# Kernel tuning notes

Measured on AMD Instinct MI355X. Metric: run time of the kernel, lower is better.

The kernel has to match this reference:

```python
import jax, jax.numpy as jnp
import numpy as np

N = 50000      # nodes
F_IN = 500     # input features
H1, C1 = 4, 32 # layer1 heads, channels (hidden)
H2, C2 = 1, 40 # layer2 heads, channels (num_classes)
E_RAW = 250000 # random edges before self loops
SLOPE = 0.2    # leaky relu negative slope


def _build_edges():
    """1-hop edges with self loops (remove_self_loops+add_self_loops) and
    unique 2-hop edges (nonzeros of adj @ adj), as ints. Deterministic."""
    rng = np.random.RandomState(0)
    src = rng.randint(0, N, E_RAW)
    dst = (src + 1 + rng.randint(0, N - 1, E_RAW)) % N  # no self loops by construction
    sl = np.arange(N)
    src1 = np.concatenate([src, sl])
    dst1 = np.concatenate([dst, sl])
    # CSR by source for 2-hop expansion
    order = np.argsort(src1, kind='stable')
    dst_sorted = dst1[order]
    deg = np.bincount(src1, minlength=N)
    ptr = np.concatenate([[0], np.cumsum(deg)])
    rep = deg[dst1]                      # continuations per edge (a,b) = outdeg(b)
    total = int(rep.sum())
    base = np.repeat(np.cumsum(rep) - rep, rep)
    off = np.arange(total) - base
    starts = np.repeat(ptr[dst1], rep)
    cont = dst_sorted[starts + off]
    two_src = np.repeat(src1, rep)
    key = two_src.astype(np.int64) * N + cont.astype(np.int64)
    uk = np.unique(key)                  # dense_to_sparse keeps unique nonzero positions
    e2 = np.stack([uk // N, uk % N]).astype(np.int32)
    e1 = np.stack([src1, dst1]).astype(np.int32)
    return e1, e2


def _glorot(k, shape):
    fan_in = int(np.prod(shape[:-1]))
    fan_out = int(shape[-1])
    lim = float(np.sqrt(6.0 / (fan_in + fan_out)))
    return jax.random.uniform(k, shape, jnp.float32, -lim, lim)


def setup_inputs() -> dict:
    key = jax.random.key(0)
    ks = jax.random.split(key, 13)
    e1, e2 = _build_edges()
    return {
        'x': jax.random.normal(ks[0], (N, F_IN), jnp.float32),
        'edge_index1': jnp.asarray(e1),
        'edge_index2': jnp.asarray(e2),
        'W_src1': _glorot(ks[1], (F_IN, H1 * C1)),
        'W_dst1': _glorot(ks[2], (F_IN, H1 * C1)),
        'W_dst21': _glorot(ks[3], (F_IN, H1 * C1)),
        'a_src1': _glorot(ks[4], (1, H1, C1)),
        'a_dst1': _glorot(ks[5], (1, H1, C1)),
        'a_dst21': _glorot(ks[6], (1, H1, C1)),
        'W_src2': _glorot(ks[7], (2 * H1 * C1, H2 * C2)),
        'W_dst2': _glorot(ks[8], (2 * H1 * C1, H2 * C2)),
        'W_dst22': _glorot(ks[9], (2 * H1 * C1, H2 * C2)),
        'a_src2': _glorot(ks[10], (1, H2, C2)),
        'a_dst2': _glorot(ks[11], (1, H2, C2)),
        'a_dst22': _glorot(ks[12], (1, H2, C2)),
    }


def _propagate(e, x_src, al_src, al_dst, n):
    """Edge gather -> leaky-relu score -> segment softmax by dst -> scatter-add."""
    s, d = e[0], e[1]
    a = al_src[s] + al_dst[d]                      # [E, H]
    a = jnp.where(a > 0, a, SLOPE * a)             # leaky relu
    amax = jax.lax.stop_gradient(jax.ops.segment_max(a, d, num_segments=n))
    a = jnp.exp(a - amax[d])
    denom = jax.ops.segment_sum(a, d, num_segments=n)
    a = a / (denom[d] + 1e-16)                     # PyG softmax epsilon
    msg = x_src[s] * a[:, :, None]                 # [E, H, C]
    return jax.ops.segment_sum(msg, d, num_segments=n)


def _gat_prop(x, e1, e2, Ws, Wd, Wd2, a_s, a_d, a_d2, H, C, concat, n):
    xs = (x @ Ws).reshape(n, H, C)
    xd = (x @ Wd).reshape(n, H, C)
    xd2 = (x @ Wd2).reshape(n, H, C)
    al_s = (xs * a_s).sum(-1)    # [N, H]
    al_d = (xd * a_d).sum(-1)
    al_d2 = (xd2 * a_d2).sum(-1)
    out = _propagate(e1, xs, al_s, al_d, n)    # 1-hop
    out2 = _propagate(e2, xs, al_s, al_d2, n)  # 2-hop
    if concat:
        out = out.reshape(n, H * C)
        out2 = out2.reshape(n, H * C)
    else:
        out = out.mean(1)
        out2 = out2.mean(1)
    return jnp.concatenate([out, out2], axis=-1)


def reference(x, edge_index1, edge_index2,
              W_src1, W_dst1, W_dst21, a_src1, a_dst1, a_dst21,
              W_src2, W_dst2, W_dst22, a_src2, a_dst2, a_dst22):
    n = x.shape[0]
    h = _gat_prop(x, edge_index1, edge_index2, W_src1, W_dst1, W_dst21,
                  a_src1, a_dst1, a_dst21, H1, C1, True, n)
    h = jax.nn.elu(h)
    h = _gat_prop(h, edge_index1, edge_index2, W_src2, W_dst2, W_dst22,
                  a_src2, a_dst2, a_dst22, H2, C2, False, n)
    return jax.nn.log_softmax(h, axis=1)
```

## Files before the change

kernel.cpp:

```cpp
#include <hip/hip_runtime.h>
#include <hip/hip_bf16.h>
#include <math.h>

typedef unsigned short u16;
typedef unsigned int u32;
typedef unsigned char u8;
typedef __attribute__((ext_vector_type(8))) short short8;
typedef __attribute__((ext_vector_type(4))) float f32x4;
typedef __attribute__((ext_vector_type(2))) float f32x2;

#define NB 128

static __device__ __forceinline__ u16 f2bf(float f) {
    u32 u = __float_as_uint(f);
    u32 r = (u + 0x7fffu + ((u >> 16) & 1u)) >> 16;
    return (u16)r;
}
static __device__ __forceinline__ float bl(u32 u) { return __uint_as_float(u << 16); }
static __device__ __forceinline__ float bh(u32 u) { return __uint_as_float(u & 0xffff0000u); }


__global__ __launch_bounds__(256) void k_bhist(const int* __restrict__ dst, int E,
                                               int* __restrict__ bcnt) {
    __shared__ int lh[NB];
    int tid = threadIdx.x;
    int base = blockIdx.x * 2048;
    for (int i = tid; i < NB; i += 256) lh[i] = 0;
    __syncthreads();
    int cnt = min(2048, E - base);
    #pragma unroll
    for (int k = 0; k < 8; k++) {
        int i = tid + k * 256;
        if (i < cnt) atomicAdd(&lh[dst[base + i] >> 9], 1);
    }
    __syncthreads();
    for (int i = tid; i < NB; i += 256) {
        int c = lh[i];
        if (c) atomicAdd(&bcnt[i], c);
    }
}

__global__ void k_bscan(const int* __restrict__ bcnt, int* __restrict__ bbase,
                        int* __restrict__ bcur, int* __restrict__ ptrN, int nb) {
    __shared__ int sh[NB];
    int t = threadIdx.x;
    int v = (t < nb) ? bcnt[t] : 0;
    sh[t] = v;
    __syncthreads();
    for (int off = 1; off < NB; off <<= 1) {
        int val = sh[t];
        int add = (t >= off) ? sh[t - off] : 0;
        __syncthreads();
        sh[t] = val + add;
        __syncthreads();
    }
    int excl = sh[t] - v;
    if (t <= nb) bbase[t] = excl;
    if (t < nb) bcur[t] = excl;
    if (t == nb) *ptrN = excl;
}

__global__ __launch_bounds__(256) void k_part(const int* __restrict__ src,
                                              const int* __restrict__ dst, int E,
                                              int* __restrict__ bcur,
                                              u32* __restrict__ part) {
    __shared__ int lh[NB];
    __shared__ int gb[NB];
    int tid = threadIdx.x;
    int base = blockIdx.x * 2048;
    for (int i = tid; i < NB; i += 256) lh[i] = 0;
    __syncthreads();
    int cnt = min(2048, E - base);
    int bkt[8], rank[8]; u32 pk[8];
    #pragma unroll
    for (int k = 0; k < 8; k++) {
        int i = tid + k * 256;
        if (i < cnt) {
            int s = src[base + i], d = dst[base + i];
            int b = d >> 9;
            bkt[k] = b;
            pk[k] = ((u32)(d & 511) << 16) | (u32)s;
            rank[k] = atomicAdd(&lh[b], 1);
        } else bkt[k] = -1;
    }
    __syncthreads();
    for (int i = tid; i < NB; i += 256) {
        int c = lh[i];
        gb[i] = c ? atomicAdd(&bcur[i], c) : 0;
    }
    __syncthreads();
    #pragma unroll
    for (int k = 0; k < 8; k++)
        if (bkt[k] >= 0) part[gb[bkt[k]] + rank[k]] = pk[k];
}

__global__ __launch_bounds__(256) void k_dhs(const u32* __restrict__ part,
                                             const int* __restrict__ bbase,
                                             int* __restrict__ ptrArr,
                                             u16* __restrict__ csr, int n) {
    __shared__ int hist[512];
    __shared__ int tsum[256];
    int b = blockIdx.x;
    int t = threadIdx.x;
    int lo = bbase[b], hi = bbase[b + 1];
    hist[t] = 0; hist[t + 256] = 0;
    __syncthreads();
    for (int i = lo + t; i < hi; i += 256)
        atomicAdd(&hist[(part[i] >> 16) & 511], 1);
    __syncthreads();
    int v0 = hist[2 * t], v1 = hist[2 * t + 1];
    tsum[t] = v0 + v1;
    __syncthreads();
    for (int off = 1; off < 256; off <<= 1) {
        int val = tsum[t];
        int add = (t >= off) ? tsum[t - off] : 0;
        __syncthreads();
        tsum[t] = val + add;
        __syncthreads();
    }
    int basep = lo + ((t == 0) ? 0 : tsum[t - 1]);
    int i0 = (b << 9) + 2 * t;
    if (i0 < n)     ptrArr[i0] = basep;
    if (i0 + 1 < n) ptrArr[i0 + 1] = basep + v0;
    __syncthreads();
    hist[2 * t] = basep;
    hist[2 * t + 1] = basep + v0;
    __syncthreads();
    for (int i = lo + t; i < hi; i += 256) {
        u32 pk = part[i];
        int pos = atomicAdd(&hist[(pk >> 16) & 511], 1);
        csr[pos] = (u16)(pk & 0xffffu);
    }
}

__global__ void k_build_Bt1(const float* __restrict__ Ws, const float* __restrict__ Wd,
                            const float* __restrict__ Wd2, const float* __restrict__ as_,
                            const float* __restrict__ ad, const float* __restrict__ ad2,
                            u16* __restrict__ Bt) {
    int t = blockIdx.x * blockDim.x + threadIdx.x;
    if (t >= 144 * 512) return;
    int nn = t >> 9, k = t & 511;
    float v = 0.f;
    if (k < 500) {
        if (nn < 128) v = Ws[k * 128 + nn];
        else if (nn < 140) {
            int q = nn - 128; int h = q & 3;
            const float* W; const float* a;
            if (q < 4)      { W = Ws;  a = as_; }
            else if (q < 8) { W = Wd;  a = ad;  }
            else            { W = Wd2; a = ad2; }
            float s = 0.f;
            #pragma unroll 8
            for (int c = 0; c < 32; c++) s += W[k * 128 + h * 32 + c] * a[h * 32 + c];
            v = s;
        }
    }
    Bt[t] = f2bf(v);
}

__global__ void k_build_Bt2(const float* __restrict__ Ws, const float* __restrict__ Wd,
                            const float* __restrict__ Wd2, const float* __restrict__ as_,
                            const float* __restrict__ ad, const float* __restrict__ ad2,
                            u16* __restrict__ Bt) {
    int t = blockIdx.x * blockDim.x + threadIdx.x;
    if (t >= 48 * 256) return;
    int nn = t >> 8, k = t & 255;
    float v = 0.f;
    if (nn < 40) v = Ws[k * 40 + nn];
    else if (nn < 43) {
        const float* a = (nn == 40) ? as_ : (nn == 41) ? ad : ad2;
        const float* W = Ws;
        if (nn == 41) W = Wd; else if (nn == 42) W = Wd2;
        float s = 0.f;
        #pragma unroll 8
        for (int c = 0; c < 40; c++) s += W[k * 40 + c] * a[c];
        v = s;
    }
    Bt[t] = f2bf(v);
}

__global__ __launch_bounds__(256) void k_mgemm1(const float* __restrict__ A,
                                                const u16* __restrict__ Bt,
                                                u8* __restrict__ xb,
                                                float* __restrict__ alb, int M) {
    __shared__ __align__(16) u16 Bs[144][136];
    int tid = threadIdx.x;
    int wv = tid >> 6, lane = tid & 63;
    int l15 = lane & 15, k8 = lane >> 4;
    int wid = blockIdx.x * 4 + wv;
    int nw = (M + 15) >> 4;
    bool active = wid < nw;
    int rowBlk = wid * 16;
    int arow = rowBlk + l15;
    bool rowOK = active && (arow < M);
    const float* Ap0 = A + (size_t)arow * 500;

    f32x4 acc[9];
    #pragma unroll
    for (int t = 0; t < 9; t++) acc[t] = (f32x4){0.f, 0.f, 0.f, 0.f};

    for (int q = 0; q < 4; q++) {
        if (q) __syncthreads();
        for (int idx = tid; idx < 2304; idx += 256) {
            int row = idx >> 4, c = (idx & 15) * 8;
            *(uint4*)&Bs[row][c] = *(const uint4*)&Bt[row * 512 + q * 128 + c];
        }
        __syncthreads();
        #pragma unroll
        for (int ki = 0; ki < 4; ki++) {
            int kg = q * 128 + ki * 32 + k8 * 8;
            float v[8];
            if (rowOK && (kg + 8 <= 500)) {
                float4 p0 = *(const float4*)(Ap0 + kg);
                float4 p1 = *(const float4*)(Ap0 + kg + 4);
                v[0] = p0.x; v[1] = p0.y; v[2] = p0.z; v[3] = p0.w;
                v[4] = p1.x; v[5] = p1.y; v[6] = p1.z; v[7] = p1.w;
            } else {
                #pragma unroll
                for (int i = 0; i < 8; i++)
                    v[i] = (rowOK && kg + i < 500) ? Ap0[kg + i] : 0.f;
            }
            short8 af;
            ((u32*)&af)[0] = (u32)f2bf(v[0]) | ((u32)f2bf(v[1]) << 16);
            ((u32*)&af)[1] = (u32)f2bf(v[2]) | ((u32)f2bf(v[3]) << 16);
            ((u32*)&af)[2] = (u32)f2bf(v[4]) | ((u32)f2bf(v[5]) << 16);
            ((u32*)&af)[3] = (u32)f2bf(v[6]) | ((u32)f2bf(v[7]) << 16);
            int kl = ki * 32 + k8 * 8;
            #pragma unroll
            for (int t = 0; t < 9; t++) {
                short8 bf = *(const short8*)&Bs[t * 16 + l15][kl];
                acc[t] = __builtin_amdgcn_mfma_f32_16x16x32_bf16(af, bf, acc[t], 0, 0, 0);
            }
        }
    }
    if (active) {
        #pragma unroll
        for (int t = 0; t < 9; t++) {
            #pragma unroll
            for (int rr = 0; rr < 4; rr++) {
                int grow = rowBlk + k8 * 4 + rr;
                if (grow < M) {
                    if (t < 8) {
                        u32 p8 = __builtin_amdgcn_cvt_pk_fp8_f32(acc[t][rr], acc[t][rr], 0, false);
                        xb[(size_t)grow * 128 + t * 16 + l15] = (u8)(p8 & 0xffu);
                    } else if (l15 < 12) {
                        alb[(size_t)grow * 16 + l15] = acc[t][rr];
                    }
                }
            }
        }
    }
}

__global__ __launch_bounds__(256) void k_mgemm2(const u16* __restrict__ A,
                                                const u16* __restrict__ Bt,
                                                u16* __restrict__ xb,
                                                float* __restrict__ alb, int M) {
    __shared__ __align__(16) u16 Bs[48][264];
    int tid = threadIdx.x;
    int wv = tid >> 6, lane = tid & 63;
    int l15 = lane & 15, k8 = lane >> 4;
    int wid = blockIdx.x * 4 + wv;
    int nw = (M + 15) >> 4;
    bool active = wid < nw;
    int rowBlk = wid * 16;
    int arow = rowBlk + l15;
    bool rowOK = active && (arow < M);
    const u16* Ap0 = A + (size_t)arow * 256;

    for (int idx = tid; idx < 1536; idx += 256) {
        int row = idx >> 5, c = (idx & 31) * 8;
        *(uint4*)&Bs[row][c] = *(const uint4*)&Bt[row * 256 + c];
    }
    __syncthreads();

    f32x4 acc[3];
    #pragma unroll
    for (int t = 0; t < 3; t++) acc[t] = (f32x4){0.f, 0.f, 0.f, 0.f};

    #pragma unroll
    for (int ki = 0; ki < 8; ki++) {
        int k0 = ki * 32 + k8 * 8;
        short8 af = {0, 0, 0, 0, 0, 0, 0, 0};
        if (rowOK) af = *(const short8*)(Ap0 + k0);
        #pragma unroll
        for (int t = 0; t < 3; t++) {
            short8 bf = *(const short8*)&Bs[t * 16 + l15][k0];
            acc[t] = __builtin_amdgcn_mfma_f32_16x16x32_bf16(af, bf, acc[t], 0, 0, 0);
        }
    }
    if (active) {
        #pragma unroll
        for (int t = 0; t < 3; t++) {
            #pragma unroll
            for (int rr = 0; rr < 4; rr++) {
                int grow = rowBlk + k8 * 4 + rr;
                if (grow < M) {
                    int col = t * 16 + l15;
                    if (col < 40) xb[(size_t)grow * 40 + col] = f2bf(acc[t][rr]);
                    else if (col < 43) alb[(size_t)grow * 4 + (col - 40)] = acc[t][rr];
                }
            }
        }
    }
}

__global__ __launch_bounds__(256) void k_prop1(const int* __restrict__ ptr, const u16* __restrict__ csr,
                                               const float* __restrict__ al, int doff,
                                               const uint2* __restrict__ xb2v,
                                               u16* __restrict__ out, int n) {
    __shared__ int sbuf[4][64];
    __shared__ __align__(16) float wbuf[4][64][4];
    int tid = threadIdx.x;
    int wv = tid >> 6, lane = tid & 63;
    int wid = (blockIdx.x * 256 + tid) >> 6;
    if (wid >= n) return;
    int b = ptr[wid], e = ptr[wid + 1];
    float4 adv = *(const float4*)(al + (size_t)wid * 16 + doff);
    int l4 = lane & 15, q = lane >> 4;
    int h = l4 >> 2;

    float acc0 = 0.f, acc1 = 0.f, acc2 = 0.f, acc3 = 0.f;
    float acc4 = 0.f, acc5 = 0.f, acc6 = 0.f, acc7 = 0.f;
    float dn0 = 0.f, dn1 = 0.f, dn2 = 0.f, dn3 = 0.f;

    for (int cb = b; cb < e; cb += 64) {
        int cnt = min(64, e - cb);
        int s = 0;
        float w0 = 0.f, w1 = 0.f, w2 = 0.f, w3 = 0.f;
        if (lane < cnt) {
            s = csr[cb + lane];
            float4 av = *(const float4*)(al + (size_t)s * 16);
            float a0 = av.x + adv.x; a0 = a0 > 0.f ? a0 : 0.2f * a0; w0 = __expf(a0);
            float a1 = av.y + adv.y; a1 = a1 > 0.f ? a1 : 0.2f * a1; w1 = __expf(a1);
            float a2 = av.z + adv.z; a2 = a2 > 0.f ? a2 : 0.2f * a2; w2 = __expf(a2);
            float a3 = av.w + adv.w; a3 = a3 > 0.f ? a3 : 0.2f * a3; w3 = __expf(a3);
        }
        dn0 += w0; dn1 += w1; dn2 += w2; dn3 += w3;
        sbuf[wv][lane] = s;
        float4 wq4; wq4.x = w0; wq4.y = w1; wq4.z = w2; wq4.w = w3;
        *(float4*)&wbuf[wv][lane][0] = wq4;
        #pragma unroll 2
        for (int j = 0; j < cnt; j += 4) {
            int jq = j + q;
            int sj = sbuf[wv][jq];
            float wj = wbuf[wv][jq][h];
            uint2 pk = xb2v[(size_t)sj * 16 + l4];
            f32x2 c01 = __builtin_amdgcn_cvt_pk_f32_fp8(pk.x, false);
            f32x2 c23 = __builtin_amdgcn_cvt_pk_f32_fp8(pk.x, true);
            f32x2 c45 = __builtin_amdgcn_cvt_pk_f32_fp8(pk.y, false);
            f32x2 c67 = __builtin_amdgcn_cvt_pk_f32_fp8(pk.y, true);
            acc0 = fmaf(wj, c01.x, acc0);
            acc1 = fmaf(wj, c01.y, acc1);
            acc2 = fmaf(wj, c23.x, acc2);
            acc3 = fmaf(wj, c23.y, acc3);
            acc4 = fmaf(wj, c45.x, acc4);
            acc5 = fmaf(wj, c45.y, acc5);
            acc6 = fmaf(wj, c67.x, acc6);
            acc7 = fmaf(wj, c67.y, acc7);
        }
    }
    acc0 += __shfl_xor(acc0, 16); acc0 += __shfl_xor(acc0, 32);
    acc1 += __shfl_xor(acc1, 16); acc1 += __shfl_xor(acc1, 32);
    acc2 += __shfl_xor(acc2, 16); acc2 += __shfl_xor(acc2, 32);
    acc3 += __shfl_xor(acc3, 16); acc3 += __shfl_xor(acc3, 32);
    acc4 += __shfl_xor(acc4, 16); acc4 += __shfl_xor(acc4, 32);
    acc5 += __shfl_xor(acc5, 16); acc5 += __shfl_xor(acc5, 32);
    acc6 += __shfl_xor(acc6, 16); acc6 += __shfl_xor(acc6, 32);
    acc7 += __shfl_xor(acc7, 16); acc7 += __shfl_xor(acc7, 32);
    #pragma unroll
    for (int o = 32; o > 0; o >>= 1) {
        dn0 += __shfl_xor(dn0, o);
        dn1 += __shfl_xor(dn1, o);
        dn2 += __shfl_xor(dn2, o);
        dn3 += __shfl_xor(dn3, o);
    }
    if (lane < 16) {
        float dh = (h == 0) ? dn0 : (h == 1) ? dn1 : (h == 2) ? dn2 : dn3;
        float inv = 1.f / (dh + 1e-16f);
        float r0 = acc0 * inv, r1 = acc1 * inv, r2 = acc2 * inv, r3 = acc3 * inv;
        float r4 = acc4 * inv, r5 = acc5 * inv, r6 = acc6 * inv, r7 = acc7 * inv;
        r0 = r0 > 0.f ? r0 : __expf(r0) - 1.f;
        r1 = r1 > 0.f ? r1 : __expf(r1) - 1.f;
        r2 = r2 > 0.f ? r2 : __expf(r2) - 1.f;
        r3 = r3 > 0.f ? r3 : __expf(r3) - 1.f;
        r4 = r4 > 0.f ? r4 : __expf(r4) - 1.f;
        r5 = r5 > 0.f ? r5 : __expf(r5) - 1.f;
        r6 = r6 > 0.f ? r6 : __expf(r6) - 1.f;
        r7 = r7 > 0.f ? r7 : __expf(r7) - 1.f;
        uint4 st;
        st.x = (u32)f2bf(r0) | ((u32)f2bf(r1) << 16);
        st.y = (u32)f2bf(r2) | ((u32)f2bf(r3) << 16);
        st.z = (u32)f2bf(r4) | ((u32)f2bf(r5) << 16);
        st.w = (u32)f2bf(r6) | ((u32)f2bf(r7) << 16);
        *(uint4*)(out + (size_t)wid * 256 + l4 * 8) = st;
    }
}

__global__ __launch_bounds__(256) void k_prop2(const int* __restrict__ ptr, const u16* __restrict__ csr,
                                               const float* __restrict__ al, int didx,
                                               const uint2* __restrict__ xbv,
                                               float* __restrict__ out, int n) {
    __shared__ int2 swb[4][64];
    int tid = threadIdx.x;
    int wv = tid >> 6, lane = tid & 63;
    int wid = (blockIdx.x * 256 + tid) >> 6;
    if (wid >= n) return;
    int b = ptr[wid], e = ptr[wid + 1];
    float ad = al[(size_t)wid * 4 + didx];
    int g = lane / 10;
    int cp = lane - g * 10;
    bool act = g < 6;

    float acc0 = 0.f, acc1 = 0.f, acc2 = 0.f, acc3 = 0.f;
    float den = 0.f;

    for (int cb = b; cb < e; cb += 64) {
        int cnt = min(64, e - cb);
        int s = 0; float w = 0.f;
        if (lane < cnt) {
            s = csr[cb + lane];
            float a = al[(size_t)s * 4] + ad;
            a = a > 0.f ? a : 0.2f * a;
            w = __expf(a);
        }
        den += w;
        swb[wv][lane] = make_int2(s, __float_as_int(w));
        #pragma unroll 2
        for (int j = 0; j < cnt; j += 6) {
            int jj = j + g;
            bool valid = act && (jj < cnt);
            int2 sw = swb[wv][valid ? jj : 0];
            float wj = valid ? __int_as_float(sw.y) : 0.f;
            uint2 pk = xbv[(size_t)sw.x * 10 + cp];
            acc0 = fmaf(wj, bl(pk.x), acc0);
            acc1 = fmaf(wj, bh(pk.x), acc1);
            acc2 = fmaf(wj, bl(pk.y), acc2);
            acc3 = fmaf(wj, bh(pk.y), acc3);
        }
    }
    float t0;
    t0 = acc0 + __shfl(acc0, (lane + 30) & 63); acc0 = t0 + __shfl(t0, (lane + 10) & 63) + __shfl(t0, (lane + 20) & 63);
    t0 = acc1 + __shfl(acc1, (lane + 30) & 63); acc1 = t0 + __shfl(t0, (lane + 10) & 63) + __shfl(t0, (lane + 20) & 63);
    t0 = acc2 + __shfl(acc2, (lane + 30) & 63); acc2 = t0 + __shfl(t0, (lane + 10) & 63) + __shfl(t0, (lane + 20) & 63);
    t0 = acc3 + __shfl(acc3, (lane + 30) & 63); acc3 = t0 + __shfl(t0, (lane + 10) & 63) + __shfl(t0, (lane + 20) & 63);
    #pragma unroll
    for (int o = 32; o > 0; o >>= 1) den += __shfl_xor(den, o);
    if (lane < 10) {
        float inv = 1.f / (den + 1e-16f);
        float4 st; st.x = acc0 * inv; st.y = acc1 * inv; st.z = acc2 * inv; st.w = acc3 * inv;
        *(float4*)(out + (size_t)wid * 80 + 4 * cp) = st;
    }
}

__global__ __launch_bounds__(256) void k_lsm(const float* __restrict__ h2, float* __restrict__ out, int n) {
    int wid = (blockIdx.x * blockDim.x + threadIdx.x) >> 6;
    int lane = threadIdx.x & 63;
    if (wid >= n) return;
    const float* row = h2 + (size_t)wid * 80;
    float v0 = row[lane];
    float v1 = (lane < 16) ? row[64 + lane] : -INFINITY;
    float m = fmaxf(v0, v1);
    for (int o = 32; o > 0; o >>= 1) m = fmaxf(m, __shfl_xor(m, o));
    float s = __expf(v0 - m) + ((lane < 16) ? __expf(v1 - m) : 0.f);
    for (int o = 32; o > 0; o >>= 1) s += __shfl_xor(s, o);
    float ls = m + logf(s);
    out[(size_t)wid * 80 + lane] = v0 - ls;
    if (lane < 16) out[(size_t)wid * 80 + 64 + lane] = v1 - ls;
}


extern "C" void kernel_launch(void* const* d_in, const int* in_sizes, int n_in,
                              void* d_out, int out_size, void* d_ws, size_t ws_size,
                              hipStream_t stream) {
    const float* x       = (const float*)d_in[0];
    const int*   e1      = (const int*)d_in[1];
    const int*   e2      = (const int*)d_in[2];
    const float* W_src1  = (const float*)d_in[3];
    const float* W_dst1  = (const float*)d_in[4];
    const float* W_dst21 = (const float*)d_in[5];
    const float* a_src1  = (const float*)d_in[6];
    const float* a_dst1  = (const float*)d_in[7];
    const float* a_dst21 = (const float*)d_in[8];
    const float* W_src2  = (const float*)d_in[9];
    const float* W_dst2  = (const float*)d_in[10];
    const float* W_dst22 = (const float*)d_in[11];
    const float* a_src2  = (const float*)d_in[12];
    const float* a_dst2  = (const float*)d_in[13];
    const float* a_dst22 = (const float*)d_in[14];
    float* out = (float*)d_out;

    const int FIN = 500;
    int n  = in_sizes[0] / FIN;
    int E1 = in_sizes[1] / 2;
    int E2 = in_sizes[2] / 2;
    const int* src1 = e1, *dst1 = e1 + E1;
    const int* src2 = e2, *dst2 = e2 + E2;
    int nb = (n + 511) >> 9;

    char* w = (char*)d_ws;
    auto alloc = [&](size_t bytes) -> char* {
        char* p = w; w += (bytes + 255) & ~(size_t)255; return p;
    };
    u8*    xb1  = (u8*)alloc((size_t)n * 128);
    float* alb1 = (float*)alloc((size_t)n * 16 * 4);
    u16*   hbuf = (u16*)alloc((size_t)n * 256 * 2);
    u16*   xb2  = (u16*)alloc((size_t)n * 40 * 2);
    float* alb2 = (float*)alloc((size_t)n * 4 * 4);
    float* h2   = (float*)alloc((size_t)n * 80 * 4);
    u16*   Bt1  = (u16*)alloc(144 * 512 * 2);
    u16*   Bt2  = (u16*)alloc(48 * 256 * 2);
    int* ptr1 = (int*)alloc((size_t)(n + 1) * 4);
    u16* csr1 = (u16*)alloc((size_t)E1 * 2);
    int* ptr2 = (int*)alloc((size_t)(n + 1) * 4);
    u16* csr2 = (u16*)alloc((size_t)E2 * 2);
    int* bcnt1  = (int*)alloc(NB * 4);
    int* bcnt2  = (int*)alloc(NB * 4);
    int* bbase1 = (int*)alloc((NB + 1) * 4);
    int* bbase2 = (int*)alloc((NB + 1) * 4);
    int* bcur1  = (int*)alloc(NB * 4);
    int* bcur2  = (int*)alloc(NB * 4);
    u32* part2 = (u32*)h2;
    u32* part1 = part2 + E2;

    hipMemsetAsync(bcnt1, 0, NB * 4, stream);
    hipMemsetAsync(bcnt2, 0, NB * 4, stream);
    k_bhist<<<(E1 + 2047) / 2048, 256, 0, stream>>>(dst1, E1, bcnt1);
    k_bhist<<<(E2 + 2047) / 2048, 256, 0, stream>>>(dst2, E2, bcnt2);
    k_bscan<<<1, NB, 0, stream>>>(bcnt1, bbase1, bcur1, ptr1 + n, nb);
    k_bscan<<<1, NB, 0, stream>>>(bcnt2, bbase2, bcur2, ptr2 + n, nb);
    k_part<<<(E1 + 2047) / 2048, 256, 0, stream>>>(src1, dst1, E1, bcur1, part1);
    k_part<<<(E2 + 2047) / 2048, 256, 0, stream>>>(src2, dst2, E2, bcur2, part2);
    k_dhs<<<nb, 256, 0, stream>>>(part1, bbase1, ptr1, csr1, n);
    k_dhs<<<nb, 256, 0, stream>>>(part2, bbase2, ptr2, csr2, n);

    k_build_Bt1<<<(144 * 512 + 255) / 256, 256, 0, stream>>>(W_src1, W_dst1, W_dst21,
                                                             a_src1, a_dst1, a_dst21, Bt1);
    int nw = (n + 15) / 16;
    k_mgemm1<<<(nw + 3) / 4, 256, 0, stream>>>(x, Bt1, xb1, alb1, n);

    int pblocks = (n + 3) / 4;
    k_prop1<<<pblocks, 256, 0, stream>>>(ptr1, csr1, alb1, 4, (const uint2*)xb1, hbuf + 0, n);
    k_prop1<<<pblocks, 256, 0, stream>>>(ptr2, csr2, alb1, 8, (const uint2*)xb1, hbuf + 128, n);

    k_build_Bt2<<<(48 * 256 + 255) / 256, 256, 0, stream>>>(W_src2, W_dst2, W_dst22,
                                                            a_src2, a_dst2, a_dst22, Bt2);
    k_mgemm2<<<(nw + 3) / 4, 256, 0, stream>>>(hbuf, Bt2, xb2, alb2, n);

    k_prop2<<<pblocks, 256, 0, stream>>>(ptr1, csr1, alb2, 1, (const uint2*)xb2, h2 + 0, n);
    k_prop2<<<pblocks, 256, 0, stream>>>(ptr2, csr2, alb2, 2, (const uint2*)xb2, h2 + 40, n);

    k_lsm<<<pblocks, 256, 0, stream>>>(h2, out, n);
}
```

Before: 292.5 us.

## Merge paired graph-build and propagation launches; split first GEMM output tiles across waves

The separate kernels for the 1-hop and 2-hop edge sets (histogram, scan, partition, CSR build, both propagation layers) and the two weight-prep kernels are each merged into one launch, choosing the data set by block or wave index. The two counter memsets become one, which relies on bcnt2 sitting directly after bcnt1 in memory. The first MFMA GEMM now gives each 16-row tile to two waves, one taking 5 output tiles and the other 4. This doubles the wave count and lowers accumulator registers per wave, at the cost of each wave converting the A rows to bf16 again. The aim is to cut launch overhead and inter-kernel gaps and to fill the GPU better in the small per-graph stages.

Measured after the change: 276.2 us. 1.06x faster.

```diff
diff --git a/kernel.cpp b/kernel.cpp
--- a/kernel.cpp
+++ b/kernel.cpp
@@ -20,11 +20,16 @@
 static __device__ __forceinline__ float bh(u32 u) { return __uint_as_float(u & 0xffff0000u); }
 
 
-__global__ __launch_bounds__(256) void k_bhist(const int* __restrict__ dst, int E,
-                                               int* __restrict__ bcnt) {
+__global__ __launch_bounds__(256) void k_bhist2(const int* __restrict__ dst1, int E1,
+                                                int* __restrict__ bcnt1,
+                                                const int* __restrict__ dst2, int E2,
+                                                int* __restrict__ bcnt2, int nblk1) {
     __shared__ int lh[NB];
+    const int* dst; int E; int* bcnt; int bb;
+    if (blockIdx.x < nblk1) { dst = dst1; E = E1; bcnt = bcnt1; bb = blockIdx.x; }
+    else                    { dst = dst2; E = E2; bcnt = bcnt2; bb = blockIdx.x - nblk1; }
     int tid = threadIdx.x;
-    int base = blockIdx.x * 2048;
+    int base = bb * 2048;
     for (int i = tid; i < NB; i += 256) lh[i] = 0;
     __syncthreads();
     int cnt = min(2048, E - base);
@@ -40,9 +45,15 @@
     }
 }
 
-__global__ void k_bscan(const int* __restrict__ bcnt, int* __restrict__ bbase,
-                        int* __restrict__ bcur, int* __restrict__ ptrN, int nb) {
+__global__ void k_bscan2(const int* __restrict__ bcnt1, int* __restrict__ bbase1,
+                         int* __restrict__ bcur1, int* __restrict__ ptrN1,
+                         const int* __restrict__ bcnt2, int* __restrict__ bbase2,
+                         int* __restrict__ bcur2, int* __restrict__ ptrN2, int nb) {
     __shared__ int sh[NB];
+    const int* bcnt = blockIdx.x ? bcnt2 : bcnt1;
+    int* bbase = blockIdx.x ? bbase2 : bbase1;
+    int* bcur  = blockIdx.x ? bcur2  : bcur1;
+    int* ptrN  = blockIdx.x ? ptrN2  : ptrN1;
     int t = threadIdx.x;
     int v = (t < nb) ? bcnt[t] : 0;
     sh[t] = v;
@@ -60,14 +71,20 @@
     if (t == nb) *ptrN = excl;
 }
 
-__global__ __launch_bounds__(256) void k_part(const int* __restrict__ src,
-                                              const int* __restrict__ dst, int E,
-                                              int* __restrict__ bcur,
-                                              u32* __restrict__ part) {
+__global__ __launch_bounds__(256) void k_part2(const int* __restrict__ src1,
+                                               const int* __restrict__ dst1, int E1,
+                                               int* __restrict__ bcur1, u32* __restrict__ part1,
+                                               const int* __restrict__ src2,
+                                               const int* __restrict__ dst2, int E2,
+                                               int* __restrict__ bcur2, u32* __restrict__ part2,
+                                               int nblk1) {
     __shared__ int lh[NB];
     __shared__ int gb[NB];
+    const int* src; const int* dst; int E; int* bcur; u32* part; int bb;
+    if (blockIdx.x < nblk1) { src = src1; dst = dst1; E = E1; bcur = bcur1; part = part1; bb = blockIdx.x; }
+    else                    { src = src2; dst = dst2; E = E2; bcur = bcur2; part = part2; bb = blockIdx.x - nblk1; }
     int tid = threadIdx.x;
-    int base = blockIdx.x * 2048;
+    int base = bb * 2048;
     for (int i = tid; i < NB; i += 256) lh[i] = 0;
     __syncthreads();
     int cnt = min(2048, E - base);
@@ -94,13 +111,19 @@
         if (bkt[k] >= 0) part[gb[bkt[k]] + rank[k]] = pk[k];
 }
 
-__global__ __launch_bounds__(256) void k_dhs(const u32* __restrict__ part,
-                                             const int* __restrict__ bbase,
-                                             int* __restrict__ ptrArr,
-                                             u16* __restrict__ csr, int n) {
+__global__ __launch_bounds__(256) void k_dhs2(const u32* __restrict__ part1,
+                                              const int* __restrict__ bbase1,
+                                              int* __restrict__ ptrA1, u16* __restrict__ csr1,
+                                              const u32* __restrict__ part2,
+                                              const int* __restrict__ bbase2,
+                                              int* __restrict__ ptrA2, u16* __restrict__ csr2,
+                                              int n, int nbk) {
     __shared__ int hist[512];
     __shared__ int tsum[256];
     int b = blockIdx.x;
+    const u32* part; const int* bbase; int* ptrArr; u16* csr;
+    if (b < nbk) { part = part1; bbase = bbase1; ptrArr = ptrA1; csr = csr1; }
+    else         { b -= nbk; part = part2; bbase = bbase2; ptrArr = ptrA2; csr = csr2; }
     int t = threadIdx.x;
     int lo = bbase[b], hi = bbase[b + 1];
     hist[t] = 0; hist[t + 256] = 0;
@@ -133,50 +156,49 @@
     }
 }
 
-__global__ void k_build_Bt1(const float* __restrict__ Ws, const float* __restrict__ Wd,
-                            const float* __restrict__ Wd2, const float* __restrict__ as_,
-                            const float* __restrict__ ad, const float* __restrict__ ad2,
-                            u16* __restrict__ Bt) {
+__global__ void k_build2(const float* __restrict__ Ws1, const float* __restrict__ Wd1,
+                         const float* __restrict__ Wd21, const float* __restrict__ as1,
+                         const float* __restrict__ ad1, const float* __restrict__ ad21,
+                         const float* __restrict__ Ws2, const float* __restrict__ Wd2,
+                         const float* __restrict__ Wd22, const float* __restrict__ as2,
+                         const float* __restrict__ ad2, const float* __restrict__ ad22,
+                         u16* __restrict__ Bt1, u16* __restrict__ Bt2) {
     int t = blockIdx.x * blockDim.x + threadIdx.x;
-    if (t >= 144 * 512) return;
-    int nn = t >> 9, k = t & 511;
-    float v = 0.f;
-    if (k < 500) {
-        if (nn < 128) v = Ws[k * 128 + nn];
-        else if (nn < 140) {
-            int q = nn - 128; int h = q & 3;
-            const float* W; const float* a;
-            if (q < 4)      { W = Ws;  a = as_; }
-            else if (q < 8) { W = Wd;  a = ad;  }
-            else            { W = Wd2; a = ad2; }
+    if (t < 144 * 512) {
+        int nn = t >> 9, k = t & 511;
+        float v = 0.f;
+        if (k < 500) {
+            if (nn < 128) v = Ws1[k * 128 + nn];
+            else if (nn < 140) {
+                int q = nn - 128; int h = q & 3;
+                const float* W; const float* a;
+                if (q < 4)      { W = Ws1;  a = as1; }
+                else if (q < 8) { W = Wd1;  a = ad1;  }
+                else            { W = Wd21; a = ad21; }
+                float s = 0.f;
+                #pragma unroll 8
+                for (int c = 0; c < 32; c++) s += W[k * 128 + h * 32 + c] * a[h * 32 + c];
+                v = s;
+            }
+        }
+        Bt1[t] = f2bf(v);
+    } else {
+        t -= 144 * 512;
+        if (t >= 48 * 256) return;
+        int nn = t >> 8, k = t & 255;
+        float v = 0.f;
+        if (nn < 40) v = Ws2[k * 40 + nn];
+        else if (nn < 43) {
+            const float* a = (nn == 40) ? as2 : (nn == 41) ? ad2 : ad22;
+            const float* W = Ws2;
+            if (nn == 41) W = Wd2; else if (nn == 42) W = Wd22;
             float s = 0.f;
             #pragma unroll 8
-            for (int c = 0; c < 32; c++) s += W[k * 128 + h * 32 + c] * a[h * 32 + c];
+            for (int c = 0; c < 40; c++) s += W[k * 40 + c] * a[c];
             v = s;
         }
-    }
-    Bt[t] = f2bf(v);
-}
-
-__global__ void k_build_Bt2(const float* __restrict__ Ws, const float* __restrict__ Wd,
-                            const float* __restrict__ Wd2, const float* __restrict__ as_,
-                            const float* __restrict__ ad, const float* __restrict__ ad2,
-                            u16* __restrict__ Bt) {
-    int t = blockIdx.x * blockDim.x + threadIdx.x;
-    if (t >= 48 * 256) return;
-    int nn = t >> 8, k = t & 255;
-    float v = 0.f;
-    if (nn < 40) v = Ws[k * 40 + nn];
-    else if (nn < 43) {
-        const float* a = (nn == 40) ? as_ : (nn == 41) ? ad : ad2;
-        const float* W = Ws;
-        if (nn == 41) W = Wd; else if (nn == 42) W = Wd2;
-        float s = 0.f;
-        #pragma unroll 8
-        for (int c = 0; c < 40; c++) s += W[k * 40 + c] * a[c];
-        v = s;
-    }
-    Bt[t] = f2bf(v);
+        Bt2[t] = f2bf(v);
+    }
 }
 
 __global__ __launch_bounds__(256) void k_mgemm1(const float* __restrict__ A,
@@ -187,17 +209,21 @@
     int tid = threadIdx.x;
     int wv = tid >> 6, lane = tid & 63;
     int l15 = lane & 15, k8 = lane >> 4;
-    int wid = blockIdx.x * 4 + wv;
+    int gwid = blockIdx.x * 4 + wv;
     int nw = (M + 15) >> 4;
-    bool active = wid < nw;
-    int rowBlk = wid * 16;
+    int tile = gwid >> 1;
+    int halfw = gwid & 1;
+    bool active = tile < nw;
+    int rowBlk = tile * 16;
     int arow = rowBlk + l15;
     bool rowOK = active && (arow < M);
     const float* Ap0 = A + (size_t)arow * 500;
-
-    f32x4 acc[9];
-    #pragma unroll
-    for (int t = 0; t < 9; t++) acc[t] = (f32x4){0.f, 0.f, 0.f, 0.f};
+    int t0 = halfw ? 5 : 0;
+    int tcnt = halfw ? 4 : 5;
+
+    f32x4 acc[5];
+    #pragma unroll
+    for (int i = 0; i < 5; i++) acc[i] = (f32x4){0.f, 0.f, 0.f, 0.f};
 
     for (int q = 0; q < 4; q++) {
         if (q) __syncthreads();
@@ -227,24 +253,29 @@
             ((u32*)&af)[3] = (u32)f2bf(v[6]) | ((u32)f2bf(v[7]) << 16);
             int kl = ki * 32 + k8 * 8;
             #pragma unroll
-            for (int t = 0; t < 9; t++) {
-                short8 bf = *(const short8*)&Bs[t * 16 + l15][kl];
-                acc[t] = __builtin_amdgcn_mfma_f32_16x16x32_bf16(af, bf, acc[t], 0, 0, 0);
+            for (int i = 0; i < 5; i++) {
+                if (i < tcnt) {
+                    short8 bf = *(const short8*)&Bs[(t0 + i) * 16 + l15][kl];
+                    acc[i] = __builtin_amdgcn_mfma_f32_16x16x32_bf16(af, bf, acc[i], 0, 0, 0);
+                }
             }
         }
     }
     if (active) {
         #pragma unroll
-        for (int t = 0; t < 9; t++) {
-            #pragma unroll
-            for (int rr = 0; rr < 4; rr++) {
-                int grow = rowBlk + k8 * 4 + rr;
-                if (grow < M) {
-                    if (t < 8) {
-                        u32 p8 = __builtin_amdgcn_cvt_pk_fp8_f32(acc[t][rr], acc[t][rr], 0, false);
-                        xb[(size_t)grow * 128 + t * 16 + l15] = (u8)(p8 & 0xffu);
-                    } else if (l15 < 12) {
-                        alb[(size_t)grow * 16 + l15] = acc[t][rr];
+        for (int i = 0; i < 5; i++) {
+            if (i < tcnt) {
+                int t = t0 + i;
+                #pragma unroll
+                for (int rr = 0; rr < 4; rr++) {
+                    int grow = rowBlk + k8 * 4 + rr;
+                    if (grow < M) {
+                        if (t < 8) {
+                            u32 p8 = __builtin_amdgcn_cvt_pk_fp8_f32(acc[i][rr], acc[i][rr], 0, false);
+                            xb[(size_t)grow * 128 + t * 16 + l15] = (u8)(p8 & 0xffu);
+                        } else if (l15 < 12) {
+                            alb[(size_t)grow * 16 + l15] = acc[i][rr];
+                        }
                     }
                 }
             }
@@ -305,18 +336,26 @@
     }
 }
 
-__global__ __launch_bounds__(256) void k_prop1(const int* __restrict__ ptr, const u16* __restrict__ csr,
-                                               const float* __restrict__ al, int doff,
-                                               const uint2* __restrict__ xb2v,
-                                               u16* __restrict__ out, int n) {
+__global__ __launch_bounds__(256) void k_prop1f(const int* __restrict__ ptr1, const u16* __restrict__ csr1,
+                                                const int* __restrict__ ptr2, const u16* __restrict__ csr2,
+                                                const float* __restrict__ al,
+                                                const uint2* __restrict__ xb2v,
+                                                u16* __restrict__ out, int n) {
     __shared__ int sbuf[4][64];
     __shared__ __align__(16) float wbuf[4][64][4];
     int tid = threadIdx.x;
     int wv = tid >> 6, lane = tid & 63;
     int wid = (blockIdx.x * 256 + tid) >> 6;
-    if (wid >= n) return;
-    int b = ptr[wid], e = ptr[wid + 1];
-    float4 adv = *(const float4*)(al + (size_t)wid * 16 + doff);
+    if (wid >= 2 * n) return;
+    bool g2 = wid >= n;
+    int node = g2 ? wid - n : wid;
+    const int* ptr = g2 ? ptr2 : ptr1;
+    const u16* csr = g2 ? csr2 : csr1;
+    int doff = g2 ? 8 : 4;
+    u16* outp = out + (size_t)node * 256 + (g2 ? 128 : 0);
+
+    int b = ptr[node], e = ptr[node + 1];
+    float4 adv = *(const float4*)(al + (size_t)node * 16 + doff);
     int l4 = lane & 15, q = lane >> 4;
     int h = l4 >> 2;
 
@@ -393,21 +432,29 @@
         st.y = (u32)f2bf(r2) | ((u32)f2bf(r3) << 16);
         st.z = (u32)f2bf(r4) | ((u32)f2bf(r5) << 16);
         st.w = (u32)f2bf(r6) | ((u32)f2bf(r7) << 16);
-        *(uint4*)(out + (size_t)wid * 256 + l4 * 8) = st;
-    }
-}
-
-__global__ __launch_bounds__(256) void k_prop2(const int* __restrict__ ptr, const u16* __restrict__ csr,
-                                               const float* __restrict__ al, int didx,
-                                               const uint2* __restrict__ xbv,
-                                               float* __restrict__ out, int n) {
+        *(uint4*)(outp + l4 * 8) = st;
+    }
+}
+
+__global__ __launch_bounds__(256) void k_prop2f(const int* __restrict__ ptr1, const u16* __restrict__ csr1,
+                                                const int* __restrict__ ptr2, const u16* __restrict__ csr2,
+                                                const float* __restrict__ al,
+                                                const uint2* __restrict__ xbv,
+                                                float* __restrict__ out, int n) {
     __shared__ int2 swb[4][64];
     int tid = threadIdx.x;
     int wv = tid >> 6, lane = tid & 63;
     int wid = (blockIdx.x * 256 + tid) >> 6;
-    if (wid >= n) return;
-    int b = ptr[wid], e = ptr[wid + 1];
-    float ad = al[(size_t)wid * 4 + didx];
+    if (wid >= 2 * n) return;
+    bool g2 = wid >= n;
+    int node = g2 ? wid - n : wid;
+    const int* ptr = g2 ? ptr2 : ptr1;
+    const u16* csr = g2 ? csr2 : csr1;
+    int didx = g2 ? 2 : 1;
+    float* outp = out + (size_t)node * 80 + (g2 ? 40 : 0);
+
+    int b = ptr[node], e = ptr[node + 1];
+    float ad = al[(size_t)node * 4 + didx];
     int g = lane / 10;
     int cp = lane - g * 10;
     bool act = g < 6;
@@ -449,7 +496,7 @@
     if (lane < 10) {
         float inv = 1.f / (den + 1e-16f);
         float4 st; st.x = acc0 * inv; st.y = acc1 * inv; st.z = acc2 * inv; st.w = acc3 * inv;
-        *(float4*)(out + (size_t)wid * 80 + 4 * cp) = st;
+        *(float4*)(outp + 4 * cp) = st;
     }
 }
 
@@ -523,32 +570,33 @@
     u32* part2 = (u32*)h2;
     u32* part1 = part2 + E2;
 
-    hipMemsetAsync(bcnt1, 0, NB * 4, stream);
-    hipMemsetAsync(bcnt2, 0, NB * 4, stream);
-    k_bhist<<<(E1 + 2047) / 2048, 256, 0, stream>>>(dst1, E1, bcnt1);
-    k_bhist<<<(E2 + 2047) / 2048, 256, 0, stream>>>(dst2, E2, bcnt2);
-    k_bscan<<<1, NB, 0, stream>>>(bcnt1, bbase1, bcur1, ptr1 + n, nb);
-    k_bscan<<<1, NB, 0, stream>>>(bcnt2, bbase2, bcur2, ptr2 + n, nb);
-    k_part<<<(E1 + 2047) / 2048, 256, 0, stream>>>(src1, dst1, E1, bcur1, part1);
-    k_part<<<(E2 + 2047) / 2048, 256, 0, stream>>>(src2, dst2, E2, bcur2, part2);
-    k_dhs<<<nb, 256, 0, stream>>>(part1, bbase1, ptr1, csr1, n);
-    k_dhs<<<nb, 256, 0, stream>>>(part2, bbase2, ptr2, csr2, n);
-
-    k_build_Bt1<<<(144 * 512 + 255) / 256, 256, 0, stream>>>(W_src1, W_dst1, W_dst21,
-                                                             a_src1, a_dst1, a_dst21, Bt1);
+    int nblk1 = (E1 + 2047) / 2048;
+    int nblk2 = (E2 + 2047) / 2048;
+
+    hipMemsetAsync(bcnt1, 0, 2 * NB * 4, stream);
+    k_bhist2<<<nblk1 + nblk2, 256, 0, stream>>>(dst1, E1, bcnt1, dst2, E2, bcnt2, nblk1);
+    k_bscan2<<<2, NB, 0, stream>>>(bcnt1, bbase1, bcur1, ptr1 + n,
+                                   bcnt2, bbase2, bcur2, ptr2 + n, nb);
+    k_part2<<<nblk1 + nblk2, 256, 0, stream>>>(src1, dst1, E1, bcur1, part1,
+                                               src2, dst2, E2, bcur2, part2, nblk1);
+    k_dhs2<<<2 * nb, 256, 0, stream>>>(part1, bbase1, ptr1, csr1,
+                                       part2, bbase2, ptr2, csr2, n, nb);
+
+    k_build2<<<(144 * 512 + 48 * 256 + 255) / 256, 256, 0, stream>>>(
+        W_src1, W_dst1, W_dst21, a_src1, a_dst1, a_dst21,
+        W_src2, W_dst2, W_dst22, a_src2, a_dst2, a_dst22, Bt1, Bt2);
+
     int nw = (n + 15) / 16;
-    k_mgemm1<<<(nw + 3) / 4, 256, 0, stream>>>(x, Bt1, xb1, alb1, n);
-
-    int pblocks = (n + 3) / 4;
-    k_prop1<<<pblocks, 256, 0, stream>>>(ptr1, csr1, alb1, 4, (const uint2*)xb1, hbuf + 0, n);
-    k_prop1<<<pblocks, 256, 0, stream>>>(ptr2, csr2, alb1, 8, (const uint2*)xb1, hbuf + 128, n);
-
-    k_build_Bt2<<<(48 * 256 + 255) / 256, 256, 0, stream>>>(W_src2, W_dst2, W_dst22,
-                                                            a_src2, a_dst2, a_dst22, Bt2);
+    k_mgemm1<<<(2 * nw + 3) / 4, 256, 0, stream>>>(x, Bt1, xb1, alb1, n);
+
+    int pblocks2 = (2 * n + 3) / 4;
+    k_prop1f<<<pblocks2, 256, 0, stream>>>(ptr1, csr1, ptr2, csr2, alb1,
+                                           (const uint2*)xb1, hbuf, n);
+
     k_mgemm2<<<(nw + 3) / 4, 256, 0, stream>>>(hbuf, Bt2, xb2, alb2, n);
 
-    k_prop2<<<pblocks, 256, 0, stream>>>(ptr1, csr1, alb2, 1, (const uint2*)xb2, h2 + 0, n);
-    k_prop2<<<pblocks, 256, 0, stream>>>(ptr2, csr2, alb2, 2, (const uint2*)xb2, h2 + 40, n);
-
-    k_lsm<<<pblocks, 256, 0, stream>>>(h2, out, n);
-}
+    k_prop2f<<<pblocks2, 256, 0, stream>>>(ptr1, csr1, ptr2, csr2, alb2,
+                                           (const uint2*)xb2, h2, n);
+
+    k_lsm<<<(n + 3) / 4, 256, 0, stream>>>(h2, out, n);
+}
```
